# Kernel optimization log

Hardware: AMD Instinct MI355X
Metric: run time of the kernel (lower is better)

Reference implementation:

```python
import jax, jax.numpy as jnp
import numpy as np

EPS = 1e-5  # PNA std-aggregator epsilon
N_NODES, N_EDGES, F_DIM, N_LAYERS = 50000, 800000, 64, 3


def setup_inputs() -> dict:
    key = jax.random.key(0)
    ks = jax.random.split(key, 6)
    x = jax.random.normal(ks[0], (N_NODES, F_DIM), jnp.float32)
    edge_index = jax.random.randint(ks[1], (2, N_EDGES), 0, N_NODES, jnp.int32)
    # Per-layer parameters, stacked on a leading layer axis.
    pre_w = jax.random.normal(ks[2], (N_LAYERS, 2 * F_DIM, F_DIM), jnp.float32) / np.sqrt(2 * F_DIM).astype(np.float32)
    pre_b = jnp.zeros((N_LAYERS, F_DIM), jnp.float32)
    post_w = jax.random.normal(ks[3], (N_LAYERS, 13 * F_DIM, F_DIM), jnp.float32) / np.sqrt(13 * F_DIM).astype(np.float32)
    post_b = jnp.zeros((N_LAYERS, F_DIM), jnp.float32)
    lin_w = jax.random.normal(ks[4], (N_LAYERS, F_DIM, F_DIM), jnp.float32) / np.sqrt(F_DIM).astype(np.float32)
    lin_b = jnpp = jnp.zeros((N_LAYERS, F_DIM), jnp.float32)
    return dict(x=x, edge_index=edge_index, pre_w=pre_w, pre_b=pre_b,
                post_w=post_w, post_b=post_b, lin_w=lin_w, lin_b=lin_b)


def reference(x, edge_index, pre_w, pre_b, post_w, post_b, lin_w, lin_b):
    src, dst = edge_index[0], edge_index[1]
    n = x.shape[0]
    # In-degree of aggregation targets (clamped to >=1, as in PyG DegreeScalerAggregation).
    deg = jax.ops.segment_sum(jnp.ones_like(dst, dtype=x.dtype), dst, num_segments=n)
    has_edge = (deg > 0)[:, None]
    deg_c = jnp.maximum(deg, 1.0)[:, None]              # [N,1]
    log_deg = jnp.log(deg_c + 1.0)                      # [N,1]
    avg_log = jnp.mean(log_deg)
    amp = log_deg / avg_log                              # amplification scaler
    att = avg_log / log_deg                              # attenuation scaler

    h = x
    for l in range(pre_w.shape[0]):
        # message: pre_nn(cat([x_i, x_j]))  -> [E, F]
        m = jnp.concatenate([h[dst], h[src]], axis=-1) @ pre_w[l] + pre_b[l]
        # fused multi-aggregator scatter-reduce per target node
        s1 = jax.ops.segment_sum(m, dst, num_segments=n)
        s2 = jax.ops.segment_sum(m * m, dst, num_segments=n)
        mean = s1 / deg_c
        std = jnp.sqrt(jax.nn.relu(s2 / deg_c - mean * mean) + EPS)
        mx = jnp.where(has_edge, jax.ops.segment_max(m, dst, num_segments=n), 0.0)
        mn = jnp.where(has_edge, jax.ops.segment_min(m, dst, num_segments=n), 0.0)
        agg = jnp.concatenate([mean, mx, mn, std], axis=-1)        # [N, 4F]
        scaled = jnp.concatenate([agg, agg * amp, agg * att], -1)  # [N, 12F]
        # post_nn(cat([x, scaled])) then final lin, plus residual shortcut
        out = jnp.concatenate([h, scaled], axis=-1) @ post_w[l] + post_b[l]
        out = out @ lin_w[l] + lin_b[l]
        h = out + h
    return h
```

## Files before the change

### kernel.cpp

```cpp
#include <hip/hip_runtime.h>
#include <math.h>

#define EPSV 1e-5f
#define EPB3 4096
#define NBP 256
#define CAP 6144
#define CAPS (CAP + 768)

typedef short s16x8 __attribute__((ext_vector_type(8)));
typedef float f32x4 __attribute__((ext_vector_type(4)));
typedef unsigned short u16;
typedef unsigned short u16x4 __attribute__((ext_vector_type(4)));

#define MFMA(a, b, c) __builtin_amdgcn_mfma_f32_16x16x32_bf16(a, b, c, 0, 0, 0)

__device__ inline u16 f2bf(float f) {
    unsigned u = __float_as_uint(f);
    return (u16)((u + 0x7FFF + ((u >> 16) & 1)) >> 16);
}
__device__ inline float bf2f(u16 h) { return __uint_as_float(((unsigned)h) << 16); }

__device__ inline void split8(const float4& a, const float4& b, s16x8& hv, s16x8& lv) {
    float f[8] = {a.x, a.y, a.z, a.w, b.x, b.y, b.z, b.w};
#pragma unroll
    for (int i = 0; i < 8; ++i) {
        u16 h = f2bf(f[i]);
        hv[i] = (short)h;
        lv[i] = (short)f2bf(f[i] - bf2f(h));
    }
}


__global__ void k_wprep(const float* __restrict__ pre_w, const float* __restrict__ post_w,
                        const float* __restrict__ post_b, const float* __restrict__ lin_w,
                        const float* __restrict__ lin_b, u16* __restrict__ WpT_hi,
                        u16* __restrict__ WpT_lo, u16* __restrict__ WT_hi,
                        u16* __restrict__ WT_lo, float* __restrict__ bpp,
                        int* __restrict__ bucketCur, float* __restrict__ lsum) {
    int l = blockIdx.y, bx = blockIdx.x, t = threadIdx.x;
    if (bx < 320) {
        int k = bx, j = t;
        int third = j >> 6, c = j & 63;
        float out = 0.f;
        int r = -1;
        if (k < 64) r = (third == 0) ? k : -1;
        else        r = 64 + third * 256 + (k - 64);
        if (r >= 0) {
            const float* pw = post_w + (size_t)(l * 832 + r) * 64;
            const float* lw = lin_w + (size_t)l * 64 * 64;
            float s = 0.f;
            for (int kk = 0; kk < 64; ++kk) s += pw[kk] * lw[kk * 64 + c];
            out = s;
        }
        u16 h = f2bf(out);
        size_t o = ((size_t)l * 192 + j) * 320 + k;
        WT_hi[o] = h;
        WT_lo[o] = f2bf(out - bf2f(h));
    } else if (bx < 448) {
        if (t < 64) {
            int c = bx - 320, k = t;
            float v = pre_w[(size_t)l * 8192 + (size_t)(k + (c >= 64 ? 64 : 0)) * 64 + (c & 63)];
            u16 h = f2bf(v);
            size_t o = ((size_t)l * 128 + c) * 64 + k;
            WpT_hi[o] = h;
            WpT_lo[o] = f2bf(v - bf2f(h));
        }
    } else if (bx == 448) {
        if (t < 64) {
            int c = t;
            const float* pb = post_b + l * 64;
            const float* lw = lin_w + (size_t)l * 64 * 64;
            float s = lin_b[l * 64 + c];
            for (int k = 0; k < 64; ++k) s += pb[k] * lw[k * 64 + c];
            bpp[l * 64 + c] = s;
        }
    } else if (l == 0) {
        int i = (bx - 449) * 192 + t;
        if (i < NBP) bucketCur[i] = 0;
        if (i == 0) *lsum = 0.f;
    }
}

__global__ __launch_bounds__(512) void k_bucket3(const int* __restrict__ src,
                                                 const int* __restrict__ dst, int E,
                                                 int* __restrict__ bucketCursor,
                                                 unsigned* __restrict__ edgeTmp) {
    __shared__ int cnt[NBP], loff[NBP], lpos[NBP], gbase[NBP], sbuf[NBP];
    __shared__ unsigned stage[EPB3];
    int t = threadIdx.x;
    int base = blockIdx.x * EPB3;
    int cntE = min(EPB3, E - base);
    if (t < NBP) cnt[t] = 0;
    __syncthreads();
    unsigned ed[8];
#pragma unroll
    for (int j = 0; j < 8; ++j) {
        int idx = j * 512 + t;
        if (idx < cntE) {
            int e = base + idx;
            unsigned s = (unsigned)src[e];
            unsigned d = (unsigned)dst[e];
            ed[j] = ((d >> 8) << 24) | ((d & 255u) << 16) | s;
            atomicAdd(&cnt[d >> 8], 1);
        } else ed[j] = 0xFFFFFFFFu;
    }
    __syncthreads();
    if (t < NBP) sbuf[t] = cnt[t];
    __syncthreads();
    for (int o = 1; o < NBP; o <<= 1) {
        int v = 0;
        if (t < NBP && t >= o) v = sbuf[t - o];
        __syncthreads();
        if (t < NBP) sbuf[t] += v;
        __syncthreads();
    }
    if (t < NBP) {
        loff[t] = sbuf[t] - cnt[t];
        lpos[t] = sbuf[t] - cnt[t];
        gbase[t] = (cnt[t] > 0) ? atomicAdd(&bucketCursor[t], cnt[t]) : 0;
    }
    __syncthreads();
#pragma unroll
    for (int j = 0; j < 8; ++j) {
        if (ed[j] != 0xFFFFFFFFu) {
            int b = ed[j] >> 24;
            int p = atomicAdd(&lpos[b], 1);
            stage[p] = ed[j];
        }
    }
    __syncthreads();
    for (int i = t; i < cntE; i += 512) {
        unsigned pr = stage[i];
        int b = pr >> 24;
        int pos = gbase[b] + (i - loff[b]);
        if (pos < CAP) edgeTmp[(size_t)b * CAP + pos] = pr;
    }
}

__global__ __launch_bounds__(512) void k_csort2(const unsigned* __restrict__ edgeTmp,
                                                const int* __restrict__ bucketCur,
                                                int* __restrict__ deg,
                                                int* __restrict__ offs,
                                                float* __restrict__ lsum,
                                                u16* __restrict__ srcSorted,
                                                int N, int E, int NB) {
    __shared__ int scnt[NBP], sbuf[NBP], lcur[NBP], lofs[NBP];
    __shared__ float fred[256];
    __shared__ u16 stageSrc[CAPS];
    __shared__ int cntPs;
    int b = blockIdx.x, t = threadIdx.x;
    int n0 = b << 8;
    int nodes = min(256, N - n0);
    if (t < NBP) { lcur[t] = 0; scnt[t] = 0; }
    __syncthreads();
    int cnt = min(bucketCur[b], CAP);
    const unsigned* ebase = edgeTmp + (size_t)b * CAP;
    for (int i = t; i < cnt; i += 512) atomicAdd(&lcur[(ebase[i] >> 16) & 255], 1);
    __syncthreads();
    float ls = 0.f;
    int d = 0, dP = 0;
    if (t < nodes) {
        d = lcur[t];
        deg[n0 + t] = d;
        ls = logf(fmaxf((float)d, 1.f) + 1.f);
        dP = (d + 3) & ~3;
    }
    if (t < 256) fred[t] = ls;
    if (t < NBP) sbuf[t] = dP;
    __syncthreads();
    for (int o = 1; o < NBP; o <<= 1) {
        int v = 0;
        if (t < NBP && t >= o) v = sbuf[t - o];
        __syncthreads();
        if (t < NBP) sbuf[t] += v;
        __syncthreads();
    }
    if (t < NBP) lofs[t] = sbuf[t] - dP;
    if (t < nodes) offs[n0 + t] = b * CAPS + (sbuf[t] - dP);
    if (t == NBP - 1) cntPs = sbuf[t];
    __syncthreads();
    for (int o = 128; o > 0; o >>= 1) {
        if (t < o) fred[t] += fred[t + o];
        __syncthreads();
    }
    if (t == 0) atomicAdd(lsum, fred[0]);
    for (int i = t; i < cnt; i += 512) {
        unsigned p = ebase[i];
        int dl = (p >> 16) & 255;
        int r = atomicAdd(&scnt[dl], 1);
        stageSrc[lofs[dl] + r] = (u16)(p & 0xFFFFu);
    }
    __syncthreads();
    if (t < nodes && (d & 3)) {
        int lp = lofs[t];
        u16 lastv = stageSrc[lp + d - 1];
        for (int k = d; k < dP; ++k) stageSrc[lp + k] = lastv;
    }
    __syncthreads();
    int cntP = cntPs;
    for (int i = t; i < cntP; i += 512) srcSorted[(size_t)b * CAPS + i] = stageSrc[i];
}


__global__ __launch_bounds__(256) void k_gemm1(const float* __restrict__ h,
                                               const u16* __restrict__ WpT_hi,
                                               const u16* __restrict__ WpT_lo,
                                               const float* __restrict__ pre_b,
                                               u16* __restrict__ Ph, u16* __restrict__ Qh,
                                               int M) {
    __shared__ u16 Ah[64 * 72], Al[64 * 72];
    __shared__ u16 Bh[128 * 72], Bl[128 * 72];
    int t = threadIdx.x, wid = t >> 6, lane = t & 63;
    int rows0 = blockIdx.x * 64;
    int quad = lane >> 4, l16 = lane & 15;
    int wm = wid & 1, wn = wid >> 1;

#pragma unroll
    for (int it = 0; it < 2; ++it) {
        int task = it * 256 + t;
        int r = task >> 3, seg = task & 7;
        int row = rows0 + r;
        float4 v0 = make_float4(0.f, 0.f, 0.f, 0.f), v1 = v0;
        if (row < M) {
            v0 = *(const float4*)&h[(size_t)row * 64 + seg * 8];
            v1 = *(const float4*)&h[(size_t)row * 64 + seg * 8 + 4];
        }
        s16x8 hv, lv;
        split8(v0, v1, hv, lv);
        *(s16x8*)&Ah[r * 72 + seg * 8] = hv;
        *(s16x8*)&Al[r * 72 + seg * 8] = lv;
    }
#pragma unroll
    for (int it = 0; it < 4; ++it) {
        int task = it * 256 + t;
        int c = task >> 3, seg = task & 7;
        *(s16x8*)&Bh[c * 72 + seg * 8] = *(const s16x8*)&WpT_hi[(size_t)c * 64 + seg * 8];
        *(s16x8*)&Bl[c * 72 + seg * 8] = *(const s16x8*)&WpT_lo[(size_t)c * 64 + seg * 8];
    }
    __syncthreads();

    f32x4 acc[2][4];
#pragma unroll
    for (int mt = 0; mt < 2; ++mt)
#pragma unroll
        for (int tt = 0; tt < 4; ++tt) acc[mt][tt] = (f32x4){0.f, 0.f, 0.f, 0.f};

#pragma unroll
    for (int c = 0; c < 2; ++c) {
        s16x8 ah[2], al[2];
#pragma unroll
        for (int mt = 0; mt < 2; ++mt) {
            int r = wm * 32 + mt * 16 + l16;
            ah[mt] = *(s16x8*)&Ah[r * 72 + c * 32 + quad * 8];
            al[mt] = *(s16x8*)&Al[r * 72 + c * 32 + quad * 8];
        }
#pragma unroll
        for (int tt = 0; tt < 4; ++tt) {
            int cc = wn * 64 + tt * 16 + l16;
            s16x8 bh = *(s16x8*)&Bh[cc * 72 + c * 32 + quad * 8];
            s16x8 bl = *(s16x8*)&Bl[cc * 72 + c * 32 + quad * 8];
#pragma unroll
            for (int mt = 0; mt < 2; ++mt) {
                acc[mt][tt] = MFMA(ah[mt], bh, acc[mt][tt]);
                acc[mt][tt] = MFMA(ah[mt], bl, acc[mt][tt]);
                if (wn == 0) acc[mt][tt] = MFMA(al[mt], bh, acc[mt][tt]);
            }
        }
    }

#pragma unroll
    for (int mt = 0; mt < 2; ++mt)
#pragma unroll
        for (int tt = 0; tt < 4; ++tt) {
            int col = wn * 64 + tt * 16 + l16;
#pragma unroll
            for (int r = 0; r < 4; ++r) {
                int row = rows0 + wm * 32 + mt * 16 + quad * 4 + r;
                if (row >= M) continue;
                float v = acc[mt][tt][r];
                if (col < 64) Ph[(size_t)row * 64 + col] = f2bf(v + pre_b[col]);
                else          Qh[(size_t)row * 64 + (col - 64)] = f2bf(v);
            }
        }
}

__global__ __launch_bounds__(256) void k_agg(const u16* __restrict__ Ph,
                                             const u16* __restrict__ Qh,
                                             const int* __restrict__ offs,
                                             const int* __restrict__ degp,
                                             const u16* __restrict__ ss,
                                             u16* __restrict__ AGGh, int N) {
    int w = threadIdx.x >> 6, lane = threadIdx.x & 63;
    int g = lane >> 4;
    int f4b = (lane & 15) << 3;
    int node = blockIdx.x * 16 + w * 4 + g;
    int nc = min(node, N - 1);
    int beg = offs[nc];
    int d = (node < N) ? degp[nc] : 0;
    int dP = (d + 3) & ~3;
    int end = beg + dP;
    int mdP = dP;
    mdP = max(mdP, __shfl_xor(mdP, 16));
    mdP = max(mdP, __shfl_xor(mdP, 32));
    int trips = mdP >> 2;

    float sum0 = 0.f, sum1 = 0.f, sum2 = 0.f, sum3 = 0.f;
    float sq0 = 0.f, sq1 = 0.f, sq2 = 0.f, sq3 = 0.f;
    float mx0 = -3.4e38f, mx1 = -3.4e38f, mx2 = -3.4e38f, mx3 = -3.4e38f;
    float mn0 = 3.4e38f, mn1 = 3.4e38f, mn2 = 3.4e38f, mn3 = 3.4e38f;

    const char* qbase = (const char*)Qh;

#define ACC4(LO, HI)                                                        \
    {                                                                       \
        float q0 = __uint_as_float((LO) << 16);                             \
        float q1 = __uint_as_float((LO) & 0xFFFF0000u);                     \
        float q2 = __uint_as_float((HI) << 16);                             \
        float q3 = __uint_as_float((HI) & 0xFFFF0000u);                     \
        sum0 += q0; sq0 = fmaf(q0, q0, sq0);                                \
        mx0 = fmaxf(mx0, q0); mn0 = fminf(mn0, q0);                         \
        sum1 += q1; sq1 = fmaf(q1, q1, sq1);                                \
        mx1 = fmaxf(mx1, q1); mn1 = fminf(mn1, q1);                         \
        sum2 += q2; sq2 = fmaf(q2, q2, sq2);                                \
        mx2 = fmaxf(mx2, q2); mn2 = fminf(mn2, q2);                         \
        sum3 += q3; sq3 = fmaf(q3, q3, sq3);                                \
        mx3 = fmaxf(mx3, q3); mn3 = fminf(mn3, q3);                         \
    }

    int e = beg;
    for (int it = 0; it < trips; ++it, e += 4) {
        if (e < end) {
            uint2 sw = *(const uint2*)(ss + e);
            unsigned a0 = ((sw.x & 0xFFFFu) << 7) | (unsigned)f4b;
            unsigned a1 = ((sw.x >> 16) << 7) | (unsigned)f4b;
            unsigned a2 = ((sw.y & 0xFFFFu) << 7) | (unsigned)f4b;
            unsigned a3 = ((sw.y >> 16) << 7) | (unsigned)f4b;
            uint2 qa = *(const uint2*)(qbase + a0);
            uint2 qb = *(const uint2*)(qbase + a1);
            uint2 qc = *(const uint2*)(qbase + a2);
            uint2 qd = *(const uint2*)(qbase + a3);
            ACC4(qa.x, qa.y);
            ACC4(qb.x, qb.y);
            ACC4(qc.x, qc.y);
            ACC4(qd.x, qd.y);
        }
    }
#undef ACC4

    if (d & 3) {
        unsigned sl = ss[beg + d - 1];
        uint2 ql = *(const uint2*)(qbase + ((sl << 7) | (unsigned)f4b));
        float padf = (float)(dP - d);
        float qL0 = __uint_as_float(ql.x << 16);
        float qL1 = __uint_as_float(ql.x & 0xFFFF0000u);
        float qL2 = __uint_as_float(ql.y << 16);
        float qL3 = __uint_as_float(ql.y & 0xFFFF0000u);
        float t0 = padf * qL0, t1 = padf * qL1, t2 = padf * qL2, t3 = padf * qL3;
        sum0 -= t0; sq0 = fmaf(-t0, qL0, sq0);
        sum1 -= t1; sq1 = fmaf(-t1, qL1, sq1);
        sum2 -= t2; sq2 = fmaf(-t2, qL2, sq2);
        sum3 -= t3; sq3 = fmaf(-t3, qL3, sq3);
    }

    float dc = fmaxf((float)d, 1.f);
    float inv = 1.0f / dc;
    float e0 = sum0 * inv, e1 = sum1 * inv, e2 = sum2 * inv, e3 = sum3 * inv;
    float sd0 = sqrtf(fmaxf(fmaf(-e0, e0, sq0 * inv), 0.f) + EPSV);
    float sd1 = sqrtf(fmaxf(fmaf(-e1, e1, sq1 * inv), 0.f) + EPSV);
    float sd2 = sqrtf(fmaxf(fmaf(-e2, e2, sq2 * inv), 0.f) + EPSV);
    float sd3 = sqrtf(fmaxf(fmaf(-e3, e3, sq3 * inv), 0.f) + EPSV);

    uint2 pw = *(const uint2*)((const char*)Ph + (((unsigned)nc << 7) | (unsigned)f4b));
    float p0 = __uint_as_float(pw.x << 16), p1 = __uint_as_float(pw.x & 0xFFFF0000u);
    float p2 = __uint_as_float(pw.y << 16), p3 = __uint_as_float(pw.y & 0xFFFF0000u);

    bool he = d > 0;
    float m0 = he ? p0 + e0 : 0.f, m1 = he ? p1 + e1 : 0.f;
    float m2 = he ? p2 + e2 : 0.f, m3 = he ? p3 + e3 : 0.f;
    float X0 = he ? p0 + mx0 : 0.f, X1 = he ? p1 + mx1 : 0.f;
    float X2 = he ? p2 + mx2 : 0.f, X3 = he ? p3 + mx3 : 0.f;
    float n0 = he ? p0 + mn0 : 0.f, n1 = he ? p1 + mn1 : 0.f;
    float n2 = he ? p2 + mn2 : 0.f, n3 = he ? p3 + mn3 : 0.f;

    if (node < N) {
        u16* out = (u16*)((char*)AGGh + (((unsigned)node << 9) | (unsigned)f4b));
        *(u16x4*)(out)       = (u16x4){f2bf(m0), f2bf(m1), f2bf(m2), f2bf(m3)};
        *(u16x4*)(out + 64)  = (u16x4){f2bf(X0), f2bf(X1), f2bf(X2), f2bf(X3)};
        *(u16x4*)(out + 128) = (u16x4){f2bf(n0), f2bf(n1), f2bf(n2), f2bf(n3)};
        *(u16x4*)(out + 192) = (u16x4){f2bf(sd0), f2bf(sd1), f2bf(sd2), f2bf(sd3)};
    }
}

__global__ __launch_bounds__(512) void k_gemm2(const float* __restrict__ hIn,
                                               const u16* __restrict__ AGGh,
                                               const u16* __restrict__ WT_hi,
                                               const u16* __restrict__ WT_lo,
                                               const float* __restrict__ bpp,
                                               const int* __restrict__ degp,
                                               const float* __restrict__ lsum,
                                               float* __restrict__ hOut,
                                               int doNext,
                                               const u16* __restrict__ WpN_hi,
                                               const u16* __restrict__ WpN_lo,
                                               const float* __restrict__ pre_bN,
                                               u16* __restrict__ PhN,
                                               u16* __restrict__ QhN, int M) {
    __shared__ u16 Ah[128 * 40], Al[128 * 40];
    __shared__ u16 Bh[192 * 40], Bl[192 * 40];
    int t = threadIdx.x, wid = t >> 6, lane = t & 63;
    int rows0 = blockIdx.x * 128;
    int quad = lane >> 4, l16 = lane & 15;
    int wm = wid & 3, wn = wid >> 2;

    f32x4 acc[2][6];
#pragma unroll
    for (int mt = 0; mt < 2; ++mt)
#pragma unroll
        for (int tt = 0; tt < 6; ++tt) acc[mt][tt] = (f32x4){0.f, 0.f, 0.f, 0.f};

#pragma unroll
    for (int chunk = 0; chunk < 2; ++chunk) {
        {
            int r = t >> 2, seg = t & 3;
            int row = rows0 + r;
            float4 v0 = make_float4(0.f, 0.f, 0.f, 0.f), v1 = v0;
            if (row < M) {
                v0 = *(const float4*)&hIn[(size_t)row * 64 + chunk * 32 + seg * 8];
                v1 = *(const float4*)&hIn[(size_t)row * 64 + chunk * 32 + seg * 8 + 4];
            }
            s16x8 hv, lv;
            split8(v0, v1, hv, lv);
            *(s16x8*)&Ah[r * 40 + seg * 8] = hv;
            *(s16x8*)&Al[r * 40 + seg * 8] = lv;
        }
        if (t < 256) {
            int c = t >> 2, seg = t & 3;
            int k0g = chunk * 32;
            *(s16x8*)&Bh[c * 40 + seg * 8] = *(const s16x8*)&WT_hi[(size_t)c * 320 + k0g + seg * 8];
            *(s16x8*)&Bl[c * 40 + seg * 8] = *(const s16x8*)&WT_lo[(size_t)c * 320 + k0g + seg * 8];
        }
        __syncthreads();

        s16x8 ah[2], al[2];
#pragma unroll
        for (int mt = 0; mt < 2; ++mt) {
            int r = wm * 32 + mt * 16 + l16;
            ah[mt] = *(s16x8*)&Ah[r * 40 + quad * 8];
            al[mt] = *(s16x8*)&Al[r * 40 + quad * 8];
        }
#pragma unroll
        for (int cg = 0; cg < 2; ++cg) {
            int cc = wn * 32 + cg * 16 + l16;
            s16x8 bh = *(s16x8*)&Bh[cc * 40 + quad * 8];
            s16x8 bl = *(s16x8*)&Bl[cc * 40 + quad * 8];
#pragma unroll
            for (int mt = 0; mt < 2; ++mt) {
                acc[mt][cg] = MFMA(ah[mt], bh, acc[mt][cg]);
                acc[mt][cg] = MFMA(al[mt], bh, acc[mt][cg]);
                acc[mt][cg] = MFMA(ah[mt], bl, acc[mt][cg]);
            }
        }
        __syncthreads();
    }

    for (int chunk = 0; chunk < 8; ++chunk) {
        {
            int r = t >> 2, seg = t & 3;
            int row = rows0 + r;
            s16x8 v = (s16x8){0, 0, 0, 0, 0, 0, 0, 0};
            if (row < M) v = *(const s16x8*)&AGGh[(size_t)row * 256 + chunk * 32 + seg * 8];
            *(s16x8*)&Ah[r * 40 + seg * 8] = v;
        }
        {
            int k0g = 64 + chunk * 32;
#pragma unroll
            for (int it = 0; it < 2; ++it) {
                int task = it * 512 + t;
                if (task < 768) {
                    int c = task >> 2, seg = task & 3;
                    *(s16x8*)&Bh[c * 40 + seg * 8] = *(const s16x8*)&WT_hi[(size_t)c * 320 + k0g + seg * 8];
                    *(s16x8*)&Bl[c * 40 + seg * 8] = *(const s16x8*)&WT_lo[(size_t)c * 320 + k0g + seg * 8];
                }
            }
        }
        __syncthreads();

        s16x8 ah[2];
#pragma unroll
        for (int mt = 0; mt < 2; ++mt) {
            int r = wm * 32 + mt * 16 + l16;
            ah[mt] = *(s16x8*)&Ah[r * 40 + quad * 8];
        }
#pragma unroll
        for (int tt = 0; tt < 6; ++tt) {
            int cc = wn * 32 + (tt & 1) * 16 + (tt >> 1) * 64 + l16;
            s16x8 bh = *(s16x8*)&Bh[cc * 40 + quad * 8];
            s16x8 bl = *(s16x8*)&Bl[cc * 40 + quad * 8];
#pragma unroll
            for (int mt = 0; mt < 2; ++mt) {
                acc[mt][tt] = MFMA(ah[mt], bh, acc[mt][tt]);
                acc[mt][tt] = MFMA(ah[mt], bl, acc[mt][tt]);
            }
        }
        __syncthreads();
    }

    float hv[2][2][4];
    float avg = *lsum / (float)M;
#pragma unroll
    for (int mt = 0; mt < 2; ++mt)
#pragma unroll
        for (int r = 0; r < 4; ++r) {
            int row = rows0 + wm * 32 + mt * 16 + quad * 4 + r;
            float am = 1.f, at = 1.f, hin0 = 0.f, hin1 = 0.f;
            if (row < M) {
                float dc = fmaxf((float)degp[row], 1.f);
                float ld = logf(dc + 1.f);
                am = ld / avg;
                at = avg / ld;
                hin0 = hIn[(size_t)row * 64 + wn * 32 + l16];
                hin1 = hIn[(size_t)row * 64 + wn * 32 + 16 + l16];
            }
#pragma unroll
            for (int cg = 0; cg < 2; ++cg) {
                int col = wn * 32 + cg * 16 + l16;
                float v = acc[mt][cg][r] + am * acc[mt][cg + 2][r] + at * acc[mt][cg + 4][r]
                        + (cg == 0 ? hin0 : hin1) + bpp[col];
                hv[mt][cg][r] = v;
                if (row < M) hOut[(size_t)row * 64 + col] = v;
            }
        }

    if (doNext) {
        f32x4 acc2[2][4];
#pragma unroll
        for (int mt = 0; mt < 2; ++mt)
#pragma unroll
            for (int tt = 0; tt < 4; ++tt) acc2[mt][tt] = (f32x4){0.f, 0.f, 0.f, 0.f};

#pragma unroll
        for (int chunk = 0; chunk < 2; ++chunk) {
            {
                int c = t >> 2, seg = t & 3;
                *(s16x8*)&Bh[c * 40 + seg * 8] = *(const s16x8*)&WpN_hi[(size_t)c * 64 + chunk * 32 + seg * 8];
                *(s16x8*)&Bl[c * 40 + seg * 8] = *(const s16x8*)&WpN_lo[(size_t)c * 64 + chunk * 32 + seg * 8];
            }
            if (wn == chunk) {
#pragma unroll
                for (int mt = 0; mt < 2; ++mt)
#pragma unroll
                    for (int cg = 0; cg < 2; ++cg) {
                        int lc = cg * 16 + l16;
#pragma unroll
                        for (int r = 0; r < 4; ++r) {
                            int rl = wm * 32 + mt * 16 + quad * 4 + r;
                            float v = hv[mt][cg][r];
                            u16 hi = f2bf(v);
                            Ah[rl * 40 + lc] = hi;
                            Al[rl * 40 + lc] = f2bf(v - bf2f(hi));
                        }
                    }
            }
            __syncthreads();

            s16x8 ah[2], al[2];
#pragma unroll
            for (int mt = 0; mt < 2; ++mt) {
                int r = wm * 32 + mt * 16 + l16;
                ah[mt] = *(s16x8*)&Ah[r * 40 + quad * 8];
                al[mt] = *(s16x8*)&Al[r * 40 + quad * 8];
            }
#pragma unroll
            for (int tt = 0; tt < 4; ++tt) {
                int cc = wn * 64 + tt * 16 + l16;
                s16x8 bh = *(s16x8*)&Bh[cc * 40 + quad * 8];
                s16x8 bl = *(s16x8*)&Bl[cc * 40 + quad * 8];
#pragma unroll
                for (int mt = 0; mt < 2; ++mt) {
                    acc2[mt][tt] = MFMA(ah[mt], bh, acc2[mt][tt]);
                    acc2[mt][tt] = MFMA(ah[mt], bl, acc2[mt][tt]);
                    if (wn == 0) acc2[mt][tt] = MFMA(al[mt], bh, acc2[mt][tt]);
                }
            }
            __syncthreads();
        }

#pragma unroll
        for (int mt = 0; mt < 2; ++mt)
#pragma unroll
            for (int tt = 0; tt < 4; ++tt) {
                int col = wn * 64 + tt * 16 + l16;
#pragma unroll
                for (int r = 0; r < 4; ++r) {
                    int row = rows0 + wm * 32 + mt * 16 + quad * 4 + r;
                    if (row >= M) continue;
                    float v = acc2[mt][tt][r];
                    if (col < 64) PhN[(size_t)row * 64 + col] = f2bf(v + pre_bN[col]);
                    else          QhN[(size_t)row * 64 + (col - 64)] = f2bf(v);
                }
            }
    }
}


extern "C" void kernel_launch(void* const* d_in, const int* in_sizes, int n_in,
                              void* d_out, int out_size, void* d_ws, size_t ws_size,
                              hipStream_t stream) {
    const float* x      = (const float*)d_in[0];
    const int*   ei     = (const int*)d_in[1];
    const float* pre_w  = (const float*)d_in[2];
    const float* pre_b  = (const float*)d_in[3];
    const float* post_w = (const float*)d_in[4];
    const float* post_b = (const float*)d_in[5];
    const float* lin_w  = (const float*)d_in[6];
    const float* lin_b  = (const float*)d_in[7];

    const int N = in_sizes[0] / 64;
    const int E = in_sizes[1] / 2;
    const int L = in_sizes[2] / (128 * 64);

    const int* srcIdx = ei;
    const int* dstIdx = ei + E;

    char* ws = (char*)d_ws;
    size_t off = 0;
    auto alloc = [&](size_t bytes) {
        void* p = ws + off;
        off += (bytes + 255) & ~(size_t)255;
        return p;
    };
    int*      deg        = (int*)alloc((size_t)N * 4);
    int*      offs       = (int*)alloc((size_t)(N + 1) * 4);
    u16*      srcSorted  = (u16*)alloc((size_t)NBP * CAPS * 2);
    unsigned* edgeTmp    = (unsigned*)alloc((size_t)NBP * CAP * 4);
    int*      bucketCur  = (int*)alloc(NBP * 4);
    float*    lsum       = (float*)alloc(256);
    u16*      WpT_hi     = (u16*)alloc((size_t)L * 128 * 64 * 2);
    u16*      WpT_lo     = (u16*)alloc((size_t)L * 128 * 64 * 2);
    u16*      WT_hi      = (u16*)alloc((size_t)L * 192 * 320 * 2);
    u16*      WT_lo      = (u16*)alloc((size_t)L * 192 * 320 * 2);
    float*    bpp        = (float*)alloc((size_t)L * 64 * 4);
    u16*      Ph         = (u16*)alloc((size_t)N * 64 * 2);
    u16*      Qh         = (u16*)alloc((size_t)N * 64 * 2);
    u16*      AGGh       = (u16*)alloc((size_t)N * 256 * 2);
    float*    hA         = (float*)alloc((size_t)N * 64 * 4);
    float*    hB         = (float*)alloc((size_t)N * 64 * 4);
    (void)ws_size;

    int NB = (N + 255) >> 8;
    int NB1 = (E + EPB3 - 1) / EPB3;
    int initBlk = (NBP + 191) / 192;

    k_wprep<<<dim3(449 + initBlk, L), 192, 0, stream>>>(
        pre_w, post_w, post_b, lin_w, lin_b, WpT_hi, WpT_lo, WT_hi, WT_lo, bpp,
        bucketCur, lsum);
    k_bucket3<<<NB1, 512, 0, stream>>>(srcIdx, dstIdx, E, bucketCur, edgeTmp);
    k_csort2<<<NB, 512, 0, stream>>>(edgeTmp, bucketCur, deg, offs, lsum,
                                     srcSorted, N, E, NB);

    int gblk = (N + 63) / 64;
    int gblk2 = (N + 127) / 128;
    k_gemm1<<<gblk, 256, 0, stream>>>(x, WpT_hi, WpT_lo, pre_b, Ph, Qh, N);

    const float* hIn = x;
    float* hbuf[2] = {hA, hB};
    for (int l = 0; l < L; ++l) {
        float* hOut = (l == L - 1) ? (float*)d_out : hbuf[l & 1];
        int dn = (l < L - 1) ? 1 : 0;
        int ln = dn ? (l + 1) : 0;
        k_agg<<<(N + 15) / 16, 256, 0, stream>>>(Ph, Qh, offs, deg, srcSorted, AGGh, N);
        k_gemm2<<<gblk2, 512, 0, stream>>>(hIn, AGGh,
                                           WT_hi + (size_t)l * 192 * 320,
                                           WT_lo + (size_t)l * 192 * 320,
                                           bpp + (size_t)l * 64,
                                           deg, lsum, hOut, dn,
                                           WpT_hi + (size_t)ln * 128 * 64,
                                           WpT_lo + (size_t)ln * 128 * 64,
                                           pre_b + (size_t)ln * 64,
                                           Ph, Qh, N);
        hIn = hOut;
    }
}
```

Baseline: 277.0 us.

## Merge preprocessing kernels into two combined launches with memset initialization

Folds weight preparation into the edge-bucketing kernel and the per-bucket counting sort into the first pre-GEMM kernel, using blockIdx ranges to pick the role of each block. Two dependent launch pairs become two heterogeneous grids, so independent work shares a wave and launch gaps and grid tails shrink. Zeroing of the bucket cursors and the log-degree sum moves to hipMemsetAsync calls. The cost is that the merged kernels share a 512-thread block size and one static shared-memory footprint of about 55 KB, which may lower occupancy for the sort blocks and leaves many weight-prep threads idle.

```diff
diff --git a/kernel.cpp b/kernel.cpp
--- a/kernel.cpp
+++ b/kernel.cpp
@@ -30,32 +30,90 @@
     }
 }
 
-
-__global__ void k_wprep(const float* __restrict__ pre_w, const float* __restrict__ post_w,
-                        const float* __restrict__ post_b, const float* __restrict__ lin_w,
-                        const float* __restrict__ lin_b, u16* __restrict__ WpT_hi,
-                        u16* __restrict__ WpT_lo, u16* __restrict__ WT_hi,
-                        u16* __restrict__ WT_lo, float* __restrict__ bpp,
-                        int* __restrict__ bucketCur, float* __restrict__ lsum) {
-    int l = blockIdx.y, bx = blockIdx.x, t = threadIdx.x;
+__global__ __launch_bounds__(512) void k_pre1(
+    const int* __restrict__ src, const int* __restrict__ dst, int E,
+    int* __restrict__ bucketCursor, unsigned* __restrict__ edgeTmp,
+    const float* __restrict__ pre_w, const float* __restrict__ post_w,
+    const float* __restrict__ post_b, const float* __restrict__ lin_w,
+    const float* __restrict__ lin_b, u16* __restrict__ WpT_hi,
+    u16* __restrict__ WpT_lo, u16* __restrict__ WT_hi, u16* __restrict__ WT_lo,
+    float* __restrict__ bpp, int NB1) {
+    __shared__ int cnt[NBP], loff[NBP], lpos[NBP], gbase[NBP], sbuf[NBP];
+    __shared__ unsigned stage[EPB3];
+    int t = threadIdx.x;
+    if ((int)blockIdx.x < NB1) {
+        int base = blockIdx.x * EPB3;
+        int cntE = min(EPB3, E - base);
+        if (t < NBP) cnt[t] = 0;
+        __syncthreads();
+        unsigned ed[8];
+#pragma unroll
+        for (int j = 0; j < 8; ++j) {
+            int idx = j * 512 + t;
+            if (idx < cntE) {
+                int e = base + idx;
+                unsigned s = (unsigned)src[e];
+                unsigned d = (unsigned)dst[e];
+                ed[j] = ((d >> 8) << 24) | ((d & 255u) << 16) | s;
+                atomicAdd(&cnt[d >> 8], 1);
+            } else ed[j] = 0xFFFFFFFFu;
+        }
+        __syncthreads();
+        if (t < NBP) sbuf[t] = cnt[t];
+        __syncthreads();
+        for (int o = 1; o < NBP; o <<= 1) {
+            int v = 0;
+            if (t < NBP && t >= o) v = sbuf[t - o];
+            __syncthreads();
+            if (t < NBP) sbuf[t] += v;
+            __syncthreads();
+        }
+        if (t < NBP) {
+            loff[t] = sbuf[t] - cnt[t];
+            lpos[t] = sbuf[t] - cnt[t];
+            gbase[t] = (cnt[t] > 0) ? atomicAdd(&bucketCursor[t], cnt[t]) : 0;
+        }
+        __syncthreads();
+#pragma unroll
+        for (int j = 0; j < 8; ++j) {
+            if (ed[j] != 0xFFFFFFFFu) {
+                int b = ed[j] >> 24;
+                int p = atomicAdd(&lpos[b], 1);
+                stage[p] = ed[j];
+            }
+        }
+        __syncthreads();
+        for (int i = t; i < cntE; i += 512) {
+            unsigned pr = stage[i];
+            int b = pr >> 24;
+            int pos = gbase[b] + (i - loff[b]);
+            if (pos < CAP) edgeTmp[(size_t)b * CAP + pos] = pr;
+        }
+        return;
+    }
+    int wq = blockIdx.x - NB1;
+    int l = wq / 449;
+    int bx = wq - l * 449;
     if (bx < 320) {
-        int k = bx, j = t;
-        int third = j >> 6, c = j & 63;
-        float out = 0.f;
-        int r = -1;
-        if (k < 64) r = (third == 0) ? k : -1;
-        else        r = 64 + third * 256 + (k - 64);
-        if (r >= 0) {
-            const float* pw = post_w + (size_t)(l * 832 + r) * 64;
-            const float* lw = lin_w + (size_t)l * 64 * 64;
-            float s = 0.f;
-            for (int kk = 0; kk < 64; ++kk) s += pw[kk] * lw[kk * 64 + c];
-            out = s;
-        }
-        u16 h = f2bf(out);
-        size_t o = ((size_t)l * 192 + j) * 320 + k;
-        WT_hi[o] = h;
-        WT_lo[o] = f2bf(out - bf2f(h));
+        if (t < 192) {
+            int k = bx, j = t;
+            int third = j >> 6, c = j & 63;
+            float out = 0.f;
+            int r = -1;
+            if (k < 64) r = (third == 0) ? k : -1;
+            else        r = 64 + third * 256 + (k - 64);
+            if (r >= 0) {
+                const float* pw = post_w + (size_t)(l * 832 + r) * 64;
+                const float* lw = lin_w + (size_t)l * 64 * 64;
+                float s = 0.f;
+                for (int kk = 0; kk < 64; ++kk) s += pw[kk] * lw[kk * 64 + c];
+                out = s;
+            }
+            u16 h = f2bf(out);
+            size_t o = ((size_t)l * 192 + j) * 320 + k;
+            WT_hi[o] = h;
+            WT_lo[o] = f2bf(out - bf2f(h));
+        }
     } else if (bx < 448) {
         if (t < 64) {
             int c = bx - 320, k = t;
@@ -65,7 +123,7 @@
             WpT_hi[o] = h;
             WpT_lo[o] = f2bf(v - bf2f(h));
         }
-    } else if (bx == 448) {
+    } else {
         if (t < 64) {
             int c = t;
             const float* pb = post_b + l * 64;
@@ -74,215 +132,158 @@
             for (int k = 0; k < 64; ++k) s += pb[k] * lw[k * 64 + c];
             bpp[l * 64 + c] = s;
         }
-    } else if (l == 0) {
-        int i = (bx - 449) * 192 + t;
-        if (i < NBP) bucketCur[i] = 0;
-        if (i == 0) *lsum = 0.f;
     }
 }
 
-__global__ __launch_bounds__(512) void k_bucket3(const int* __restrict__ src,
-                                                 const int* __restrict__ dst, int E,
-                                                 int* __restrict__ bucketCursor,
-                                                 unsigned* __restrict__ edgeTmp) {
-    __shared__ int cnt[NBP], loff[NBP], lpos[NBP], gbase[NBP], sbuf[NBP];
-    __shared__ unsigned stage[EPB3];
+__global__ __launch_bounds__(512) void k_pre2(
+    const unsigned* __restrict__ edgeTmp, const int* __restrict__ bucketCur,
+    int* __restrict__ deg, int* __restrict__ offs, float* __restrict__ lsum,
+    u16* __restrict__ srcSorted,
+    const float* __restrict__ x, const u16* __restrict__ WpT_hi,
+    const u16* __restrict__ WpT_lo, const float* __restrict__ pre_b,
+    u16* __restrict__ Ph, u16* __restrict__ Qh,
+    int N, int E, int NB) {
+    __shared__ __align__(16) char smem[55296];
     int t = threadIdx.x;
-    int base = blockIdx.x * EPB3;
-    int cntE = min(EPB3, E - base);
-    if (t < NBP) cnt[t] = 0;
-    __syncthreads();
-    unsigned ed[8];
-#pragma unroll
-    for (int j = 0; j < 8; ++j) {
-        int idx = j * 512 + t;
-        if (idx < cntE) {
-            int e = base + idx;
-            unsigned s = (unsigned)src[e];
-            unsigned d = (unsigned)dst[e];
-            ed[j] = ((d >> 8) << 24) | ((d & 255u) << 16) | s;
-            atomicAdd(&cnt[d >> 8], 1);
-        } else ed[j] = 0xFFFFFFFFu;
-    }
-    __syncthreads();
-    if (t < NBP) sbuf[t] = cnt[t];
-    __syncthreads();
-    for (int o = 1; o < NBP; o <<= 1) {
-        int v = 0;
-        if (t < NBP && t >= o) v = sbuf[t - o];
-        __syncthreads();
-        if (t < NBP) sbuf[t] += v;
-        __syncthreads();
-    }
-    if (t < NBP) {
-        loff[t] = sbuf[t] - cnt[t];
-        lpos[t] = sbuf[t] - cnt[t];
-        gbase[t] = (cnt[t] > 0) ? atomicAdd(&bucketCursor[t], cnt[t]) : 0;
-    }
-    __syncthreads();
-#pragma unroll
-    for (int j = 0; j < 8; ++j) {
-        if (ed[j] != 0xFFFFFFFFu) {
-            int b = ed[j] >> 24;
-            int p = atomicAdd(&lpos[b], 1);
-            stage[p] = ed[j];
-        }
-    }
-    __syncthreads();
-    for (int i = t; i < cntE; i += 512) {
-        unsigned pr = stage[i];
-        int b = pr >> 24;
-        int pos = gbase[b] + (i - loff[b]);
-        if (pos < CAP) edgeTmp[(size_t)b * CAP + pos] = pr;
-    }
-}
-
-__global__ __launch_bounds__(512) void k_csort2(const unsigned* __restrict__ edgeTmp,
-                                                const int* __restrict__ bucketCur,
-                                                int* __restrict__ deg,
-                                                int* __restrict__ offs,
-                                                float* __restrict__ lsum,
-                                                u16* __restrict__ srcSorted,
-                                                int N, int E, int NB) {
-    __shared__ int scnt[NBP], sbuf[NBP], lcur[NBP], lofs[NBP];
-    __shared__ float fred[256];
-    __shared__ u16 stageSrc[CAPS];
-    __shared__ int cntPs;
-    int b = blockIdx.x, t = threadIdx.x;
-    int n0 = b << 8;
-    int nodes = min(256, N - n0);
-    if (t < NBP) { lcur[t] = 0; scnt[t] = 0; }
-    __syncthreads();
-    int cnt = min(bucketCur[b], CAP);
-    const unsigned* ebase = edgeTmp + (size_t)b * CAP;
-    for (int i = t; i < cnt; i += 512) atomicAdd(&lcur[(ebase[i] >> 16) & 255], 1);
-    __syncthreads();
-    float ls = 0.f;
-    int d = 0, dP = 0;
-    if (t < nodes) {
-        d = lcur[t];
-        deg[n0 + t] = d;
-        ls = logf(fmaxf((float)d, 1.f) + 1.f);
-        dP = (d + 3) & ~3;
-    }
-    if (t < 256) fred[t] = ls;
-    if (t < NBP) sbuf[t] = dP;
-    __syncthreads();
-    for (int o = 1; o < NBP; o <<= 1) {
-        int v = 0;
-        if (t < NBP && t >= o) v = sbuf[t - o];
-        __syncthreads();
-        if (t < NBP) sbuf[t] += v;
-        __syncthreads();
-    }
-    if (t < NBP) lofs[t] = sbuf[t] - dP;
-    if (t < nodes) offs[n0 + t] = b * CAPS + (sbuf[t] - dP);
-    if (t == NBP - 1) cntPs = sbuf[t];
-    __syncthreads();
-    for (int o = 128; o > 0; o >>= 1) {
-        if (t < o) fred[t] += fred[t + o];
-        __syncthreads();
-    }
-    if (t == 0) atomicAdd(lsum, fred[0]);
-    for (int i = t; i < cnt; i += 512) {
-        unsigned p = ebase[i];
-        int dl = (p >> 16) & 255;
-        int r = atomicAdd(&scnt[dl], 1);
-        stageSrc[lofs[dl] + r] = (u16)(p & 0xFFFFu);
-    }
-    __syncthreads();
-    if (t < nodes && (d & 3)) {
-        int lp = lofs[t];
-        u16 lastv = stageSrc[lp + d - 1];
-        for (int k = d; k < dP; ++k) stageSrc[lp + k] = lastv;
-    }
-    __syncthreads();
-    int cntP = cntPs;
-    for (int i = t; i < cntP; i += 512) srcSorted[(size_t)b * CAPS + i] = stageSrc[i];
-}
-
-
-__global__ __launch_bounds__(256) void k_gemm1(const float* __restrict__ h,
-                                               const u16* __restrict__ WpT_hi,
-                                               const u16* __restrict__ WpT_lo,
-                                               const float* __restrict__ pre_b,
-                                               u16* __restrict__ Ph, u16* __restrict__ Qh,
-                                               int M) {
-    __shared__ u16 Ah[64 * 72], Al[64 * 72];
-    __shared__ u16 Bh[128 * 72], Bl[128 * 72];
-    int t = threadIdx.x, wid = t >> 6, lane = t & 63;
-    int rows0 = blockIdx.x * 64;
+    if ((int)blockIdx.x < NB) {
+        int* scnt = (int*)smem;
+        int* sbuf = (int*)(smem + 1024);
+        int* lcur = (int*)(smem + 2048);
+        int* lofs = (int*)(smem + 3072);
+        float* fred = (float*)(smem + 4096);
+        u16* stageSrc = (u16*)(smem + 5120);
+        int* cntPs = (int*)(smem + 5120 + CAPS * 2);
+        int b = blockIdx.x;
+        int n0 = b << 8;
+        int nodes = min(256, N - n0);
+        if (t < NBP) { lcur[t] = 0; scnt[t] = 0; }
+        __syncthreads();
+        int cnt = min(bucketCur[b], CAP);
+        const unsigned* ebase = edgeTmp + (size_t)b * CAP;
+        for (int i = t; i < cnt; i += 512) atomicAdd(&lcur[(ebase[i] >> 16) & 255], 1);
+        __syncthreads();
+        float ls = 0.f;
+        int d = 0, dP = 0;
+        if (t < nodes) {
+            d = lcur[t];
+            deg[n0 + t] = d;
+            ls = logf(fmaxf((float)d, 1.f) + 1.f);
+            dP = (d + 3) & ~3;
+        }
+        if (t < 256) fred[t] = ls;
+        if (t < NBP) sbuf[t] = dP;
+        __syncthreads();
+        for (int o = 1; o < NBP; o <<= 1) {
+            int v = 0;
+            if (t < NBP && t >= o) v = sbuf[t - o];
+            __syncthreads();
+            if (t < NBP) sbuf[t] += v;
+            __syncthreads();
+        }
+        if (t < NBP) lofs[t] = sbuf[t] - dP;
+        if (t < nodes) offs[n0 + t] = b * CAPS + (sbuf[t] - dP);
+        if (t == NBP - 1) *cntPs = sbuf[t];
+        __syncthreads();
+        for (int o = 128; o > 0; o >>= 1) {
+            if (t < o) fred[t] += fred[t + o];
+            __syncthreads();
+        }
+        if (t == 0) atomicAdd(lsum, fred[0]);
+        for (int i = t; i < cnt; i += 512) {
+            unsigned p = ebase[i];
+            int dl = (p >> 16) & 255;
+            int r = atomicAdd(&scnt[dl], 1);
+            stageSrc[lofs[dl] + r] = (u16)(p & 0xFFFFu);
+        }
+        __syncthreads();
+        if (t < nodes && (d & 3)) {
+            int lp = lofs[t];
+            u16 lastv = stageSrc[lp + d - 1];
+            for (int k = d; k < dP; ++k) stageSrc[lp + k] = lastv;
+        }
+        __syncthreads();
+        int cntP = *cntPs;
+        for (int i = t; i < cntP; i += 512) srcSorted[(size_t)b * CAPS + i] = stageSrc[i];
+        return;
+    }
+    u16* Ah = (u16*)smem;
+    u16* Al = (u16*)(smem + 9216);
+    u16* Bh = (u16*)(smem + 18432);
+    u16* Bl = (u16*)(smem + 36864);
+    int rows0 = ((int)blockIdx.x - NB) * 64;
+    int wid = t >> 6, lane = t & 63;
     int quad = lane >> 4, l16 = lane & 15;
     int wm = wid & 1, wn = wid >> 1;
-
-#pragma unroll
-    for (int it = 0; it < 2; ++it) {
-        int task = it * 256 + t;
-        int r = task >> 3, seg = task & 7;
-        int row = rows0 + r;
-        float4 v0 = make_float4(0.f, 0.f, 0.f, 0.f), v1 = v0;
-        if (row < M) {
-            v0 = *(const float4*)&h[(size_t)row * 64 + seg * 8];
-            v1 = *(const float4*)&h[(size_t)row * 64 + seg * 8 + 4];
-        }
-        s16x8 hv, lv;
-        split8(v0, v1, hv, lv);
-        *(s16x8*)&Ah[r * 72 + seg * 8] = hv;
-        *(s16x8*)&Al[r * 72 + seg * 8] = lv;
-    }
-#pragma unroll
-    for (int it = 0; it < 4; ++it) {
-        int task = it * 256 + t;
-        int c = task >> 3, seg = task & 7;
-        *(s16x8*)&Bh[c * 72 + seg * 8] = *(const s16x8*)&WpT_hi[(size_t)c * 64 + seg * 8];
-        *(s16x8*)&Bl[c * 72 + seg * 8] = *(const s16x8*)&WpT_lo[(size_t)c * 64 + seg * 8];
+    if (t < 256) {
+#pragma unroll
+        for (int it = 0; it < 2; ++it) {
+            int task = it * 256 + t;
+            int r = task >> 3, seg = task & 7;
+            int row = rows0 + r;
+            float4 v0 = make_float4(0.f, 0.f, 0.f, 0.f), v1 = v0;
+            if (row < N) {
+                v0 = *(const float4*)&x[(size_t)row * 64 + seg * 8];
+                v1 = *(const float4*)&x[(size_t)row * 64 + seg * 8 + 4];
+            }
+            s16x8 hv, lv;
+            split8(v0, v1, hv, lv);
+            *(s16x8*)&Ah[r * 72 + seg * 8] = hv;
+            *(s16x8*)&Al[r * 72 + seg * 8] = lv;
+        }
+#pragma unroll
+        for (int it = 0; it < 4; ++it) {
+            int task = it * 256 + t;
+            int c = task >> 3, seg = task & 7;
+            *(s16x8*)&Bh[c * 72 + seg * 8] = *(const s16x8*)&WpT_hi[(size_t)c * 64 + seg * 8];
+            *(s16x8*)&Bl[c * 72 + seg * 8] = *(const s16x8*)&WpT_lo[(size_t)c * 64 + seg * 8];
+        }
     }
     __syncthreads();
-
-    f32x4 acc[2][4];
-#pragma unroll
-    for (int mt = 0; mt < 2; ++mt)
-#pragma unroll
-        for (int tt = 0; tt < 4; ++tt) acc[mt][tt] = (f32x4){0.f, 0.f, 0.f, 0.f};
-
-#pragma unroll
-    for (int c = 0; c < 2; ++c) {
-        s16x8 ah[2], al[2];
-#pragma unroll
-        for (int mt = 0; mt < 2; ++mt) {
-            int r = wm * 32 + mt * 16 + l16;
-            ah[mt] = *(s16x8*)&Ah[r * 72 + c * 32 + quad * 8];
-            al[mt] = *(s16x8*)&Al[r * 72 + c * 32 + quad * 8];
-        }
-#pragma unroll
-        for (int tt = 0; tt < 4; ++tt) {
-            int cc = wn * 64 + tt * 16 + l16;
-            s16x8 bh = *(s16x8*)&Bh[cc * 72 + c * 32 + quad * 8];
-            s16x8 bl = *(s16x8*)&Bl[cc * 72 + c * 32 + quad * 8];
+    if (t < 256) {
+        f32x4 acc[2][4];
+#pragma unroll
+        for (int mt = 0; mt < 2; ++mt)
+#pragma unroll
+            for (int tt = 0; tt < 4; ++tt) acc[mt][tt] = (f32x4){0.f, 0.f, 0.f, 0.f};
+#pragma unroll
+        for (int c = 0; c < 2; ++c) {
+            s16x8 ah[2], al[2];
 #pragma unroll
             for (int mt = 0; mt < 2; ++mt) {
-                acc[mt][tt] = MFMA(ah[mt], bh, acc[mt][tt]);
-                acc[mt][tt] = MFMA(ah[mt], bl, acc[mt][tt]);
-                if (wn == 0) acc[mt][tt] = MFMA(al[mt], bh, acc[mt][tt]);
-            }
-        }
-    }
-
-#pragma unroll
-    for (int mt = 0; mt < 2; ++mt)
-#pragma unroll
-        for (int tt = 0; tt < 4; ++tt) {
-            int col = wn * 64 + tt * 16 + l16;
-#pragma unroll
-            for (int r = 0; r < 4; ++r) {
-                int row = rows0 + wm * 32 + mt * 16 + quad * 4 + r;
-                if (row >= M) continue;
-                float v = acc[mt][tt][r];
-                if (col < 64) Ph[(size_t)row * 64 + col] = f2bf(v + pre_b[col]);
-                else          Qh[(size_t)row * 64 + (col - 64)] = f2bf(v);
-            }
-        }
+                int r = wm * 32 + mt * 16 + l16;
+                ah[mt] = *(s16x8*)&Ah[r * 72 + c * 32 + quad * 8];
+                al[mt] = *(s16x8*)&Al[r * 72 + c * 32 + quad * 8];
+            }
+#pragma unroll
+            for (int tt = 0; tt < 4; ++tt) {
+                int cc = wn * 64 + tt * 16 + l16;
+                s16x8 bh = *(s16x8*)&Bh[cc * 72 + c * 32 + quad * 8];
+                s16x8 bl = *(s16x8*)&Bl[cc * 72 + c * 32 + quad * 8];
+#pragma unroll
+                for (int mt = 0; mt < 2; ++mt) {
+                    acc[mt][tt] = MFMA(ah[mt], bh, acc[mt][tt]);
+                    acc[mt][tt] = MFMA(ah[mt], bl, acc[mt][tt]);
+                    if (wn == 0) acc[mt][tt] = MFMA(al[mt], bh, acc[mt][tt]);
+                }
+            }
+        }
+#pragma unroll
+        for (int mt = 0; mt < 2; ++mt)
+#pragma unroll
+            for (int tt = 0; tt < 4; ++tt) {
+                int col = wn * 64 + tt * 16 + l16;
+#pragma unroll
+                for (int r = 0; r < 4; ++r) {
+                    int row = rows0 + wm * 32 + mt * 16 + quad * 4 + r;
+                    if (row >= N) continue;
+                    float v = acc[mt][tt][r];
+                    if (col < 64) Ph[(size_t)row * 64 + col] = f2bf(v + pre_b[col]);
+                    else          Qh[(size_t)row * 64 + (col - 64)] = f2bf(v);
+                }
+            }
+    }
 }
+
 
 __global__ __launch_bounds__(256) void k_agg(const u16* __restrict__ Ph,
                                              const u16* __restrict__ Qh,
@@ -649,18 +650,20 @@
 
     int NB = (N + 255) >> 8;
     int NB1 = (E + EPB3 - 1) / EPB3;
-    int initBlk = (NBP + 191) / 192;
-
-    k_wprep<<<dim3(449 + initBlk, L), 192, 0, stream>>>(
-        pre_w, post_w, post_b, lin_w, lin_b, WpT_hi, WpT_lo, WT_hi, WT_lo, bpp,
-        bucketCur, lsum);
-    k_bucket3<<<NB1, 512, 0, stream>>>(srcIdx, dstIdx, E, bucketCur, edgeTmp);
-    k_csort2<<<NB, 512, 0, stream>>>(edgeTmp, bucketCur, deg, offs, lsum,
-                                     srcSorted, N, E, NB);
-
     int gblk = (N + 63) / 64;
     int gblk2 = (N + 127) / 128;
-    k_gemm1<<<gblk, 256, 0, stream>>>(x, WpT_hi, WpT_lo, pre_b, Ph, Qh, N);
+
+    hipMemsetAsync(bucketCur, 0, NBP * 4, stream);
+    hipMemsetAsync(lsum, 0, 4, stream);
+
+    k_pre1<<<NB1 + 449 * L, 512, 0, stream>>>(
+        srcIdx, dstIdx, E, bucketCur, edgeTmp,
+        pre_w, post_w, post_b, lin_w, lin_b,
+        WpT_hi, WpT_lo, WT_hi, WT_lo, bpp, NB1);
+
+    k_pre2<<<NB + gblk, 512, 0, stream>>>(
+        edgeTmp, bucketCur, deg, offs, lsum, srcSorted,
+        x, WpT_hi, WpT_lo, pre_b, Ph, Qh, N, E, NB);
 
     const float* hIn = x;
     float* hbuf[2] = {hA, hB};
```

Result: faster. 268.3 us (-3.2%).
